# Performance work log

Hardware: AMD Instinct MI355X
Metric: run time of the kernel (lower is better)

The kernel has to match this reference:

```python
import jax, jax.numpy as jnp
import numpy as np

B, N, E, H = 2, 50000, 400000, 128


def _lin_init(k, fan_in, fan_out):
    s = 1.0 / np.sqrt(fan_in)
    kw, kb = jax.random.split(k)
    W = jax.random.uniform(kw, (fan_in, fan_out), jnp.float32, -s, s)
    b = jax.random.uniform(kb, (fan_out,), jnp.float32, -s, s)
    return W, b


def setup_inputs() -> dict:
    key = jax.random.key(0)
    ks = jax.random.split(key, 7)
    x = jax.random.normal(ks[0], (B, N, H), jnp.float32)
    edge_index = jax.random.randint(ks[1], (2, E), 0, N, jnp.int64)
    edge_attr = jax.random.normal(ks[2], (B, E, H), jnp.float32)
    We1, be1 = _lin_init(ks[3], 3 * H, H)
    We2, be2 = _lin_init(ks[4], H, H)
    Wn1, bn1 = _lin_init(ks[5], 2 * H, H)
    Wn2, bn2 = _lin_init(ks[6], H, H)
    return dict(x=x, edge_index=edge_index, edge_attr=edge_attr,
                We1=We1, be1=be1, We2=We2, be2=be2,
                Wn1=Wn1, bn1=bn1, Wn2=Wn2, bn2=bn2)


def reference(x, edge_index, edge_attr, We1, be1, We2, be2, Wn1, bn1, Wn2, bn2):
    src = edge_index[0]
    dest = edge_index[1]
    # edge model: MLP(concat(src_feat, dest_feat, edge_attr))  [B,E,3H] -> [B,E,H]
    m = jnp.concatenate([x[:, src], x[:, dest], edge_attr], axis=-1)
    e = jax.nn.relu(m @ We1 + be1) @ We2 + be2
    # node model: scatter-sum messages to dest nodes, then MLP(concat(x, agg))
    agg = jax.vmap(lambda eb: jax.ops.segment_sum(eb, dest, num_segments=x.shape[1]))(e)
    h = jnp.concatenate([x, agg], axis=-1)  # [B,N,2H]
    x_out = jax.nn.relu(h @ Wn1 + bn1) @ Wn2 + bn2
    return x_out, e
```

## Files before the change

kernel.cpp:

```cpp
#include <hip/hip_runtime.h>
#include <hip/hip_bf16.h>

#define Hd 128
#define Nn 50000
#define Ee 400000
#define Bb 2
#define NROWS 100000
#define TPB2 3125
#define NT2 6250

typedef __attribute__((ext_vector_type(8))) short bf16x8;
typedef __attribute__((ext_vector_type(4))) short bf16x4;
typedef __attribute__((ext_vector_type(4))) float f32x4;

static __device__ __forceinline__ short f2bf(float f) {
    __hip_bfloat16 h = __float2bfloat16(f);
    return *reinterpret_cast<short*>(&h);
}
static __device__ __forceinline__ float bf2f(short s) {
    union { unsigned u; float f; } v; v.u = ((unsigned)(unsigned short)s) << 16;
    return v.f;
}
static __device__ __forceinline__ bf16x8 cvt8(float4 a, float4 b) {
    bf16x8 r;
    r[0] = f2bf(a.x); r[1] = f2bf(a.y); r[2] = f2bf(a.z); r[3] = f2bf(a.w);
    r[4] = f2bf(b.x); r[5] = f2bf(b.y); r[6] = f2bf(b.z); r[7] = f2bf(b.w);
    return r;
}
static __device__ __forceinline__ unsigned pk2(float a, float b) {
    return (unsigned)(unsigned short)f2bf(a) | ((unsigned)(unsigned short)f2bf(b) << 16);
}
static __device__ __forceinline__ void lds_barrier() {
    asm volatile("s_waitcnt lgkmcnt(0)" ::: "memory");
    __builtin_amdgcn_s_barrier();
}

__global__ void prep_weights(const float* __restrict__ We1, const float* __restrict__ We2,
                             const float* __restrict__ Wn1, const float* __restrict__ Wn2,
                             short* __restrict__ wbuf) {
    int gid = blockIdx.x * 256 + threadIdx.x;
    if (gid < 32768) {
        int c = gid >> 7, k = gid & 127;
        float v = (c < 128) ? We1[k * 128 + c] : We1[(k + 128) * 128 + (c - 128)];
        wbuf[gid] = f2bf(v); return;
    }
    int g = gid - 32768;
    if (g < 16384) { int c = g >> 7, k = g & 127; wbuf[gid] = f2bf(We1[(k + 256) * 128 + c]); return; }
    g -= 16384;
    if (g < 16384) { int c = g >> 7, k = g & 127; wbuf[gid] = f2bf(We2[k * 128 + c]); return; }
    g -= 16384;
    if (g < 32768) { int c = g >> 8, k = g & 255; wbuf[gid] = f2bf(Wn1[k * 128 + c]); return; }
    g -= 32768;
    if (g < 16384) { int c = g >> 7, k = g & 127; wbuf[gid] = f2bf(Wn2[k * 128 + c]); }
}

__global__ void hist_kernel(const int* __restrict__ ei, int* __restrict__ cnt) {
    int t = blockIdx.x * 256 + threadIdx.x;
    if (t < Ee) atomicAdd(&cnt[ei[Ee + t]], 1);
}
__global__ void scan1(const int* __restrict__ cnt, int* __restrict__ cur, int* __restrict__ part) {
    __shared__ int s[256];
    int i = blockIdx.x * 256 + threadIdx.x;
    int v = (i < Nn) ? cnt[i] : 0;
    s[threadIdx.x] = v; __syncthreads();
    #pragma unroll
    for (int off = 1; off < 256; off <<= 1) {
        int u = (threadIdx.x >= off) ? s[threadIdx.x - off] : 0;
        __syncthreads(); s[threadIdx.x] += u; __syncthreads();
    }
    if (i < Nn) cur[i] = s[threadIdx.x] - v;
    if (threadIdx.x == 255) part[blockIdx.x] = s[255];
}
__global__ void scan2(int* __restrict__ part) {
    if (threadIdx.x == 0 && blockIdx.x == 0) {
        int run = 0;
        for (int i = 0; i < 196; i++) { int t = part[i]; part[i] = run; run += t; }
    }
}
__global__ void scan3(int* __restrict__ cur, const int* __restrict__ part) {
    int i = blockIdx.x * 256 + threadIdx.x;
    if (i < Nn) cur[i] += part[blockIdx.x];
}
__global__ void scatter_k(const int* __restrict__ ei, int* __restrict__ cur, int* __restrict__ elist) {
    int t = blockIdx.x * 256 + threadIdx.x;
    if (t < Ee) { int d = ei[Ee + t]; int pos = atomicAdd(&cur[d], 1); elist[pos] = t; }
}

__global__ __launch_bounds__(256) void node_pre(
    const float* __restrict__ x, const short* __restrict__ WabT,
    short* __restrict__ xa, short* __restrict__ xb)
{
    __shared__ __align__(16) short X[32 * 128];

    const int nbase = blockIdx.x * 32;
    const int t = threadIdx.x;
    const int wv = t >> 6, lane = t & 63;
    const int row16 = lane & 15, kg = lane >> 4;

    {
        int g = t >> 3, q = t & 7;
        const float* src = x + ((size_t)(nbase + g)) * Hd + q * 16;
        float4 a0 = ((const float4*)src)[0], a1 = ((const float4*)src)[1];
        float4 a2 = ((const float4*)src)[2], a3 = ((const float4*)src)[3];
        ((bf16x8*)X)[g * 16 + ((q * 2) ^ (g & 7))]     = cvt8(a0, a1);
        ((bf16x8*)X)[g * 16 + ((q * 2 + 1) ^ (g & 7))] = cvt8(a2, a3);
    }

    bf16x8 wf[4][4];
    #pragma unroll
    for (int nt = 0; nt < 4; nt++) {
        int n = wv * 64 + nt * 16 + row16;
        #pragma unroll
        for (int kt = 0; kt < 4; kt++)
            wf[kt][nt] = *(const bf16x8*)(WabT + n * 128 + kt * 32 + kg * 8);
    }
    __syncthreads();

    f32x4 acc[2][4];
    #pragma unroll
    for (int mt = 0; mt < 2; mt++)
        #pragma unroll
        for (int nt = 0; nt < 4; nt++) acc[mt][nt] = (f32x4){0.f,0.f,0.f,0.f};

    #pragma unroll
    for (int mt = 0; mt < 2; mt++) {
        int row = mt * 16 + row16;
        #pragma unroll
        for (int kt = 0; kt < 4; kt++) {
            bf16x8 xf = ((const bf16x8*)X)[row * 16 + ((kt * 4 + kg) ^ (row & 7))];
            #pragma unroll
            for (int nt = 0; nt < 4; nt++)
                acc[mt][nt] = __builtin_amdgcn_mfma_f32_16x16x32_bf16(wf[kt][nt], xf, acc[mt][nt], 0, 0, 0);
        }
    }

    #pragma unroll
    for (int mt = 0; mt < 2; mt++) {
        size_t node = nbase + mt * 16 + row16;
        #pragma unroll
        for (int nt = 0; nt < 4; nt++) {
            int ch = wv * 64 + nt * 16 + kg * 4;
            uint2 pk = { pk2(acc[mt][nt][0], acc[mt][nt][1]), pk2(acc[mt][nt][2], acc[mt][nt][3]) };
            short* dst = (ch < 128) ? (xa + node * Hd + ch) : (xb + node * Hd + (ch - 128));
            *(uint2*)dst = pk;
        }
    }
}

__global__ __launch_bounds__(512) void edge_mlp(
    const float* __restrict__ ea, const int* __restrict__ ei,
    const int* __restrict__ elist,
    const short* __restrict__ xa, const short* __restrict__ xb,
    const short* __restrict__ W1cT, const float* __restrict__ be1,
    const short* __restrict__ W2T, const float* __restrict__ be2,
    float* __restrict__ e_out, float* __restrict__ agg)
{
    __shared__ __align__(16) char smem[65536 + 1536];
    short* Aea = (short*)smem;
    short* A2  = (short*)(smem + 32768);
    int* ol = (int*)(smem + 65536);
    int* sl = ol + 128;
    int* dl = sl + 128;

    const int tile = blockIdx.x;
    const int b = tile / TPB2;
    const int w0 = (tile % TPB2) * 128;
    const int t = threadIdx.x;
    const int wv = t >> 6, lane = t & 63;
    const int row16 = lane & 15, kg = lane >> 4;
    const int n0 = wv * 16 + kg * 4;
    const int sr = t >> 3, sq = t & 7;

    if (t < 128) {
        int o = elist[w0 + t];
        ol[t] = o; sl[t] = ei[o]; dl[t] = ei[Ee + o];
    }
    __syncthreads();

    int on[8], sn[8], dn[8];
    #pragma unroll
    for (int mt = 0; mt < 8; mt++) {
        int r = mt * 16 + row16;
        on[mt] = ol[r]; sn[mt] = sl[r]; dn[mt] = dl[r];
    }

    #pragma unroll
    for (int h = 0; h < 2; h++) {
        int row = sr + h * 64;
        const float* src = ea + ((size_t)b * Ee + ol[row]) * Hd + sq * 16;
        float4 a0 = ((const float4*)src)[0], a1 = ((const float4*)src)[1];
        float4 a2 = ((const float4*)src)[2], a3 = ((const float4*)src)[3];
        ((bf16x8*)Aea)[row * 16 + ((sq * 2) ^ (row & 7))]     = cvt8(a0, a1);
        ((bf16x8*)Aea)[row * 16 + ((sq * 2 + 1) ^ (row & 7))] = cvt8(a2, a3);
    }

    bf16x8 w1[4], w2[4];
    {
        const short* wp1 = W1cT + (wv * 16 + row16) * 128 + kg * 8;
        const short* wp2 = W2T  + (wv * 16 + row16) * 128 + kg * 8;
        #pragma unroll
        for (int kt = 0; kt < 4; kt++) {
            w1[kt] = *(const bf16x8*)(wp1 + kt * 32);
            w2[kt] = *(const bf16x8*)(wp2 + kt * 32);
        }
    }
    bf16x4 av[8], bv[8];
    #pragma unroll
    for (int mt = 0; mt < 8; mt++) {
        av[mt] = *(const bf16x4*)(xa + ((size_t)b * Nn + sn[mt]) * Hd + n0);
        bv[mt] = *(const bf16x4*)(xb + ((size_t)b * Nn + dn[mt]) * Hd + n0);
    }
    const float4 b1v = *(const float4*)(be1 + n0);
    const float4 b2v = *(const float4*)(be2 + n0);
    lds_barrier();

    f32x4 acc[8];
    #pragma unroll
    for (int mt = 0; mt < 8; mt++) acc[mt] = (f32x4){0.f,0.f,0.f,0.f};
    #pragma unroll
    for (int kt = 0; kt < 4; kt++) {
        #pragma unroll
        for (int mt = 0; mt < 8; mt++) {
            int row = mt * 16 + row16;
            bf16x8 af = ((const bf16x8*)Aea)[row * 16 + ((kt * 4 + kg) ^ (row & 7))];
            acc[mt] = __builtin_amdgcn_mfma_f32_16x16x32_bf16(w1[kt], af, acc[mt], 0, 0, 0);
        }
    }

    #pragma unroll
    for (int mt = 0; mt < 8; mt++) {
        int row = mt * 16 + row16;
        float vv[4];
        #pragma unroll
        for (int r = 0; r < 4; r++) {
            float u = acc[mt][r] + b1v[r] + bf2f(av[mt][r]) + bf2f(bv[mt][r]);
            vv[r] = u > 0.f ? u : 0.f;
        }
        int G = (n0 >> 3) ^ (row & 7);
        *(uint2*)((char*)A2 + row * 256 + G * 16 + (n0 & 7) * 2) =
            (uint2){ pk2(vv[0], vv[1]), pk2(vv[2], vv[3]) };
    }
    lds_barrier();

    f32x4 acc2[8];
    #pragma unroll
    for (int mt = 0; mt < 8; mt++) acc2[mt] = (f32x4){0.f,0.f,0.f,0.f};
    #pragma unroll
    for (int kt = 0; kt < 4; kt++) {
        #pragma unroll
        for (int mt = 0; mt < 8; mt++) {
            int row = mt * 16 + row16;
            bf16x8 hf = *(const bf16x8*)((const char*)A2 + row * 256 + (((kt * 4 + kg) ^ (row & 7)) * 16));
            acc2[mt] = __builtin_amdgcn_mfma_f32_16x16x32_bf16(w2[kt], hf, acc2[mt], 0, 0, 0);
        }
    }

    float ev[8][4];
    #pragma unroll
    for (int mt = 0; mt < 8; mt++) {
        #pragma unroll
        for (int r = 0; r < 4; r++) ev[mt][r] = acc2[mt][r] + ((const float*)&b2v)[r];
        float4 ov = { ev[mt][0], ev[mt][1], ev[mt][2], ev[mt][3] };
        *(float4*)(e_out + ((size_t)b * Ee + on[mt]) * Hd + n0) = ov;
    }
    lds_barrier();

    #pragma unroll
    for (int mt = 0; mt < 8; mt++) {
        int row = mt * 16 + row16;
        float4 ov = { ev[mt][0], ev[mt][1], ev[mt][2], ev[mt][3] };
        *(float4*)(smem + row * 512 + (((n0 >> 2) ^ (row & 7)) << 4)) = ov;
    }
    lds_barrier();

    {
        int c = t & 127, rg = t >> 7;
        int g_c = c >> 2, sub = (c & 3) << 2;
        int base = rg * 32;
        float s = 0.f;
        int pd = dl[base];
        #pragma unroll
        for (int i = 0; i < 32; i++) {
            int row = base + i;
            float v = *(const float*)(smem + row * 512 + (((g_c) ^ (row & 7)) << 4) + sub);
            int d = dl[row];
            if (d != pd) {
                unsafeAtomicAdd(agg + ((size_t)b * Nn + pd) * Hd + c, s);
                s = 0.f; pd = d;
            }
            s += v;
        }
        unsafeAtomicAdd(agg + ((size_t)b * Nn + pd) * Hd + c, s);
    }
}

__global__ __launch_bounds__(512, 4) void node_mlp(
    const float* __restrict__ x, const float* __restrict__ agg,
    const short* __restrict__ Wn1T, const float* __restrict__ bn1,
    const short* __restrict__ Wn2T, const float* __restrict__ bn2,
    float* __restrict__ xout)
{
    __shared__ __align__(16) short A[32 * 256];
    __shared__ __align__(16) short A2[32 * 128];

    const int tilesPerB = (Nn + 31) / 32;
    const int bid = blockIdx.x;
    const int b = bid / tilesPerB;
    const int nbase = (bid % tilesPerB) * 32;
    const int t = threadIdx.x;
    const int wv = t >> 6, lane = t & 63;
    const int row16 = lane & 15, kg = lane >> 4;
    const int n0 = wv * 16 + kg * 4;

    {
        int g = t >> 4, q2 = t & 15;
        int n = nbase + g;
        float4 xv0 = {0,0,0,0}, xv1 = xv0;
        float4 s0 = {0,0,0,0}, s1 = s0;
        if (n < Nn) {
            const float* xr = x + ((size_t)b * Nn + n) * Hd + q2 * 8;
            xv0 = ((const float4*)xr)[0]; xv1 = ((const float4*)xr)[1];
            const float* ar = agg + ((size_t)b * Nn + n) * Hd + q2 * 8;
            s0 = ((const float4*)ar)[0]; s1 = ((const float4*)ar)[1];
        }
        ((bf16x8*)A)[g * 32 + (q2 ^ (g & 7))]        = cvt8(xv0, xv1);
        ((bf16x8*)A)[g * 32 + ((16 + q2) ^ (g & 7))] = cvt8(s0, s1);
    }

    bf16x8 w1[8];
    {
        const short* wp = Wn1T + (wv * 16 + row16) * 256 + kg * 8;
        #pragma unroll
        for (int kt = 0; kt < 8; kt++) w1[kt] = *(const bf16x8*)(wp + kt * 32);
    }
    __syncthreads();

    f32x4 acc[2];
    acc[0] = (f32x4){0.f,0.f,0.f,0.f}; acc[1] = (f32x4){0.f,0.f,0.f,0.f};
    #pragma unroll
    for (int kt = 0; kt < 8; kt++) {
        #pragma unroll
        for (int mt = 0; mt < 2; mt++) {
            int row = mt * 16 + row16;
            bf16x8 af = ((const bf16x8*)A)[row * 32 + ((kt * 4 + kg) ^ (row & 7))];
            acc[mt] = __builtin_amdgcn_mfma_f32_16x16x32_bf16(w1[kt], af, acc[mt], 0, 0, 0);
        }
    }

    float4 b1v = *(const float4*)(bn1 + n0);
    bf16x8 w2[4];
    {
        const short* wp = Wn2T + (wv * 16 + row16) * 128 + kg * 8;
        #pragma unroll
        for (int kt = 0; kt < 4; kt++) w2[kt] = *(const bf16x8*)(wp + kt * 32);
    }

    #pragma unroll
    for (int mt = 0; mt < 2; mt++) {
        int row = mt * 16 + row16;
        float v[4];
        #pragma unroll
        for (int r = 0; r < 4; r++) {
            float u = acc[mt][r] + b1v[r];
            v[r] = u > 0.f ? u : 0.f;
        }
        int G = (n0 >> 3) ^ (row & 7);
        *(uint2*)((char*)A2 + row * 256 + G * 16 + (n0 & 7) * 2) = (uint2){ pk2(v[0], v[1]), pk2(v[2], v[3]) };
    }
    __syncthreads();

    f32x4 acc2[2];
    acc2[0] = (f32x4){0.f,0.f,0.f,0.f}; acc2[1] = (f32x4){0.f,0.f,0.f,0.f};
    #pragma unroll
    for (int kt = 0; kt < 4; kt++) {
        #pragma unroll
        for (int mt = 0; mt < 2; mt++) {
            int row = mt * 16 + row16;
            bf16x8 hf = *(const bf16x8*)((const char*)A2 + row * 256 + (((kt * 4 + kg) ^ (row & 7)) * 16));
            acc2[mt] = __builtin_amdgcn_mfma_f32_16x16x32_bf16(w2[kt], hf, acc2[mt], 0, 0, 0);
        }
    }
    float4 b2v = *(const float4*)(bn2 + n0);
    #pragma unroll
    for (int mt = 0; mt < 2; mt++) {
        int node = nbase + mt * 16 + row16;
        if (node < Nn) {
            float4 ov;
            ov.x = acc2[mt][0] + b2v.x;
            ov.y = acc2[mt][1] + b2v.y;
            ov.z = acc2[mt][2] + b2v.z;
            ov.w = acc2[mt][3] + b2v.w;
            *(float4*)(xout + ((size_t)b * Nn + node) * Hd + n0) = ov;
        }
    }
}

extern "C" void kernel_launch(void* const* d_in, const int* in_sizes, int n_in,
                              void* d_out, int out_size, void* d_ws, size_t ws_size,
                              hipStream_t stream) {
    const float* x   = (const float*)d_in[0];
    const int*   ei  = (const int*)d_in[1];
    const float* ea  = (const float*)d_in[2];
    const float* We1 = (const float*)d_in[3];
    const float* be1 = (const float*)d_in[4];
    const float* We2 = (const float*)d_in[5];
    const float* be2 = (const float*)d_in[6];
    const float* Wn1 = (const float*)d_in[7];
    const float* bn1 = (const float*)d_in[8];
    const float* Wn2 = (const float*)d_in[9];
    const float* bn2 = (const float*)d_in[10];

    float* xout  = (float*)d_out;
    float* e_out = xout + (size_t)Bb * Nn * Hd;

    char* w = (char*)d_ws;
    short* wbuf  = (short*)w;
    short* xa    = (short*)(w + 229376);
    short* xb    = xa + (size_t)NROWS * Hd;
    float* agg   = (float*)(xb + (size_t)NROWS * Hd);
    int*   cnt   = (int*)(agg + (size_t)Bb * Nn * Hd);
    int*   cur   = cnt + Nn;
    int*   part  = cur + Nn;
    int*   elist = part + 256;

    hipMemsetAsync(cnt, 0, Nn * sizeof(int), stream);
    hipMemsetAsync(agg, 0, (size_t)Bb * Nn * Hd * sizeof(float), stream);

    prep_weights<<<448, 256, 0, stream>>>(We1, We2, Wn1, Wn2, wbuf);
    hist_kernel<<<(Ee + 255) / 256, 256, 0, stream>>>(ei, cnt);
    scan1<<<196, 256, 0, stream>>>(cnt, cur, part);
    scan2<<<1, 64, 0, stream>>>(part);
    scan3<<<196, 256, 0, stream>>>(cur, part);
    scatter_k<<<(Ee + 255) / 256, 256, 0, stream>>>(ei, cur, elist);

    node_pre<<<NROWS / 32, 256, 0, stream>>>(x, wbuf, xa, xb);

    edge_mlp<<<NT2, 512, 0, stream>>>(
        ea, ei, elist, xa, xb, wbuf + 32768, be1, wbuf + 49152, be2, e_out, agg);

    node_mlp<<<Bb * ((Nn + 31) / 32), 512, 0, stream>>>(
        x, agg, wbuf + 65536, bn1, wbuf + 98304, bn2, xout);
}
```

Baseline: 454.8 us.

## Halve edge_mlp LDS by reusing one buffer and staging messages as bf16

The edge kernel now reuses a single 32 KB LDS buffer for the edge-attribute tile, the hidden activations and the output staging, instead of two 32 KB buffers. It adds one extra barrier and asks for higher occupancy via launch bounds (512, 8). The messages staged for the scatter-sum are now stored in LDS as bf16 rather than fp32, which lowers the precision of the aggregated values. The aim is more resident blocks per CU to hide gather latency, at the cost of an extra sync and rounding in agg.

```diff
diff --git a/kernel.cpp b/kernel.cpp
--- a/kernel.cpp
+++ b/kernel.cpp
@@ -147,7 +147,7 @@
     }
 }
 
-__global__ __launch_bounds__(512) void edge_mlp(
+__global__ __launch_bounds__(512, 8) void edge_mlp(
     const float* __restrict__ ea, const int* __restrict__ ei,
     const int* __restrict__ elist,
     const short* __restrict__ xa, const short* __restrict__ xb,
@@ -155,10 +155,9 @@
     const short* __restrict__ W2T, const float* __restrict__ be2,
     float* __restrict__ e_out, float* __restrict__ agg)
 {
-    __shared__ __align__(16) char smem[65536 + 1536];
-    short* Aea = (short*)smem;
-    short* A2  = (short*)(smem + 32768);
-    int* ol = (int*)(smem + 65536);
+    __shared__ __align__(16) char smem[32768 + 1536];
+    short* Abuf = (short*)smem;
+    int* ol = (int*)(smem + 32768);
     int* sl = ol + 128;
     int* dl = sl + 128;
 
@@ -190,8 +189,8 @@
         const float* src = ea + ((size_t)b * Ee + ol[row]) * Hd + sq * 16;
         float4 a0 = ((const float4*)src)[0], a1 = ((const float4*)src)[1];
         float4 a2 = ((const float4*)src)[2], a3 = ((const float4*)src)[3];
-        ((bf16x8*)Aea)[row * 16 + ((sq * 2) ^ (row & 7))]     = cvt8(a0, a1);
-        ((bf16x8*)Aea)[row * 16 + ((sq * 2 + 1) ^ (row & 7))] = cvt8(a2, a3);
+        ((bf16x8*)Abuf)[row * 16 + ((sq * 2) ^ (row & 7))]     = cvt8(a0, a1);
+        ((bf16x8*)Abuf)[row * 16 + ((sq * 2 + 1) ^ (row & 7))] = cvt8(a2, a3);
     }
 
     bf16x8 w1[4], w2[4];
@@ -222,10 +221,11 @@
         #pragma unroll
         for (int mt = 0; mt < 8; mt++) {
             int row = mt * 16 + row16;
-            bf16x8 af = ((const bf16x8*)Aea)[row * 16 + ((kt * 4 + kg) ^ (row & 7))];
+            bf16x8 af = ((const bf16x8*)Abuf)[row * 16 + ((kt * 4 + kg) ^ (row & 7))];
             acc[mt] = __builtin_amdgcn_mfma_f32_16x16x32_bf16(w1[kt], af, acc[mt], 0, 0, 0);
         }
     }
+    lds_barrier();
 
     #pragma unroll
     for (int mt = 0; mt < 8; mt++) {
@@ -237,7 +237,7 @@
             vv[r] = u > 0.f ? u : 0.f;
         }
         int G = (n0 >> 3) ^ (row & 7);
-        *(uint2*)((char*)A2 + row * 256 + G * 16 + (n0 & 7) * 2) =
+        *(uint2*)((char*)Abuf + row * 256 + G * 16 + (n0 & 7) * 2) =
             (uint2){ pk2(vv[0], vv[1]), pk2(vv[2], vv[3]) };
     }
     lds_barrier();
@@ -250,17 +250,16 @@
         #pragma unroll
         for (int mt = 0; mt < 8; mt++) {
             int row = mt * 16 + row16;
-            bf16x8 hf = *(const bf16x8*)((const char*)A2 + row * 256 + (((kt * 4 + kg) ^ (row & 7)) * 16));
+            bf16x8 hf = *(const bf16x8*)((const char*)Abuf + row * 256 + (((kt * 4 + kg) ^ (row & 7)) * 16));
             acc2[mt] = __builtin_amdgcn_mfma_f32_16x16x32_bf16(w2[kt], hf, acc2[mt], 0, 0, 0);
         }
     }
 
-    float ev[8][4];
     #pragma unroll
     for (int mt = 0; mt < 8; mt++) {
-        #pragma unroll
-        for (int r = 0; r < 4; r++) ev[mt][r] = acc2[mt][r] + ((const float*)&b2v)[r];
-        float4 ov = { ev[mt][0], ev[mt][1], ev[mt][2], ev[mt][3] };
+        acc2[mt][0] += b2v.x; acc2[mt][1] += b2v.y;
+        acc2[mt][2] += b2v.z; acc2[mt][3] += b2v.w;
+        float4 ov = { acc2[mt][0], acc2[mt][1], acc2[mt][2], acc2[mt][3] };
         *(float4*)(e_out + ((size_t)b * Ee + on[mt]) * Hd + n0) = ov;
     }
     lds_barrier();
@@ -268,21 +267,22 @@
     #pragma unroll
     for (int mt = 0; mt < 8; mt++) {
         int row = mt * 16 + row16;
-        float4 ov = { ev[mt][0], ev[mt][1], ev[mt][2], ev[mt][3] };
-        *(float4*)(smem + row * 512 + (((n0 >> 2) ^ (row & 7)) << 4)) = ov;
+        int G = (n0 >> 3) ^ (row & 7);
+        *(uint2*)((char*)Abuf + row * 256 + G * 16 + (n0 & 7) * 2) =
+            (uint2){ pk2(acc2[mt][0], acc2[mt][1]), pk2(acc2[mt][2], acc2[mt][3]) };
     }
     lds_barrier();
 
     {
-        int c = t & 127, rg = t >> 7;
-        int g_c = c >> 2, sub = (c & 3) << 2;
-        int base = rg * 32;
+        int c = t & 127, rg2 = t >> 7;
+        int gc = c >> 3, sub = (c & 7) * 2;
+        int base = rg2 * 32;
         float s = 0.f;
         int pd = dl[base];
         #pragma unroll
         for (int i = 0; i < 32; i++) {
             int row = base + i;
-            float v = *(const float*)(smem + row * 512 + (((g_c) ^ (row & 7)) << 4) + sub);
+            float v = bf2f(*(const short*)((const char*)Abuf + row * 256 + ((gc ^ (row & 7)) << 4) + sub));
             int d = dl[row];
             if (d != pd) {
                 unsafeAtomicAdd(agg + ((size_t)b * Nn + pd) * Hd + c, s);
```

Measured after the change: 742.5 us. 1.63x slower.
